# Kernel optimization log

Hardware: AMD Instinct MI355X
Metric: run time of the kernel (lower is better)

## Reference

```python
import jax, jax.numpy as jnp
import numpy as np

IMAGE_SIZE = 256
PSIZE = 6
STRIDE = 2
WINDOW = IMAGE_SIZE + 1 - PSIZE  # 251
CUR = np.arange(0, WINDOW, STRIDE)
if CUR[-1] != WINDOW - 1:
    CUR = np.concatenate([CUR, np.array([WINDOW - 1])])
NPOS = len(CUR)  # 126 strided window positions per axis
BATCH = 128


def setup_inputs() -> dict:
    key = jax.random.key(0)
    x = jax.random.normal(key, (BATCH, 1, IMAGE_SIZE, IMAGE_SIZE), dtype=jnp.float32)
    return {"x": x}


def reference(x):
    # Equivalent to patch_tf.forward(to_patch): for each strided window position
    # (r, c) in CUR x CUR and each in-patch offset (i, j) in [0, PSIZE)^2,
    # output[b, r*NPOS + c, i*PSIZE + j] = x[b, 0, r + i, c + j].
    cur = jnp.asarray(CUR, dtype=jnp.int32)          # [NPOS]
    off = jnp.arange(PSIZE, dtype=jnp.int32)         # [PSIZE]
    row_idx = cur[:, None] + off[None, :]            # [NPOS, PSIZE]
    col_idx = cur[:, None] + off[None, :]            # [NPOS, PSIZE]
    img = x[:, 0]                                    # [B, H, W]
    # Advanced-index gather -> [B, NPOS, NPOS, PSIZE, PSIZE]
    patches = img[:, row_idx[:, None, :, None], col_idx[None, :, None, :]]
    return patches.reshape(x.shape[0], NPOS * NPOS, PSIZE * PSIZE)
```

## Files before the change

kernel.cpp:

```cpp
#include <hip/hip_runtime.h>


#define IMG 256
#define PSZ 6
#define NPOS 126
#define BATCHN 128
#define PATCH_ELEMS (PSZ * PSZ)
#define PER_BATCH (NPOS * NPOS * PATCH_ELEMS)
#define TOTAL_ELEMS (BATCHN * PER_BATCH)
#define TOTAL_VEC4 (TOTAL_ELEMS / 4)

__global__ __launch_bounds__(256) void image2patch_kernel(
    const float* __restrict__ x, float* __restrict__ out) {
  const int tid4 = blockIdx.x * blockDim.x + threadIdx.x;
  const int flat = tid4 * 4;

  const int b   = flat / PER_BATCH;
  const int rem = flat - b * PER_BATCH;
  const int p   = rem / PATCH_ELEMS;
  const int k   = rem - p * PATCH_ELEMS;
  const int i   = p / NPOS;
  const int j   = p - i * NPOS;

  const float* img = x + (size_t)b * (IMG * IMG) + (2 * i) * IMG + (2 * j);

  float4 v;
  {
    int kk = k;     int r = kk / PSZ, c = kk - PSZ * r; v.x = img[r * IMG + c];
    kk = k + 1;     r = kk / PSZ;     c = kk - PSZ * r; v.y = img[r * IMG + c];
    kk = k + 2;     r = kk / PSZ;     c = kk - PSZ * r; v.z = img[r * IMG + c];
    kk = k + 3;     r = kk / PSZ;     c = kk - PSZ * r; v.w = img[r * IMG + c];
  }
  reinterpret_cast<float4*>(out)[tid4] = v;
}

extern "C" void kernel_launch(void* const* d_in, const int* in_sizes, int n_in,
                              void* d_out, int out_size, void* d_ws, size_t ws_size,
                              hipStream_t stream) {
  const float* x = (const float*)d_in[0];
  float* out = (float*)d_out;
  image2patch_kernel<<<TOTAL_VEC4 / 256, 256, 0, stream>>>(x, out);
}
```

Baseline: 357.9 us.

## Stage six-row image band in LDS per output row and gather patches from shared memory

Each block now handles one (batch, window-row) pair and cooperatively loads the six input rows it needs into padded shared memory using vectorized float4 loads. Patch elements are then gathered from LDS and written as contiguous float4 stores. This replaces redundant scattered global reads with one coalesced band load per block. It adds a barrier and LDS traffic, and the per-block work no longer divides evenly among the threads.

```diff
diff --git a/kernel.cpp b/kernel.cpp
--- a/kernel.cpp
+++ b/kernel.cpp
@@ -5,33 +5,42 @@
 #define PSZ 6
 #define NPOS 126
 #define BATCHN 128
-#define PATCH_ELEMS (PSZ * PSZ)
-#define PER_BATCH (NPOS * NPOS * PATCH_ELEMS)
-#define TOTAL_ELEMS (BATCHN * PER_BATCH)
-#define TOTAL_VEC4 (TOTAL_ELEMS / 4)
+#define LDSW 257
+#define VECS_PER_BAND 1134
 
 __global__ __launch_bounds__(256) void image2patch_kernel(
     const float* __restrict__ x, float* __restrict__ out) {
-  const int tid4 = blockIdx.x * blockDim.x + threadIdx.x;
-  const int flat = tid4 * 4;
+  __shared__ float tile[PSZ * LDSW];
 
-  const int b   = flat / PER_BATCH;
-  const int rem = flat - b * PER_BATCH;
-  const int p   = rem / PATCH_ELEMS;
-  const int k   = rem - p * PATCH_ELEMS;
-  const int i   = p / NPOS;
-  const int j   = p - i * NPOS;
+  const int blk = blockIdx.x;
+  const int b = blk / NPOS;
+  const int i = blk - b * NPOS;
+  const int t = threadIdx.x;
 
-  const float* img = x + (size_t)b * (IMG * IMG) + (2 * i) * IMG + (2 * j);
+  const float* src = x + (size_t)b * (IMG * IMG) + (size_t)(2 * i) * IMG;
+  for (int idx = t; idx < PSZ * (IMG / 4); idx += 256) {
+    const int row  = idx >> 6;
+    const int col4 = idx & 63;
+    float4 v = reinterpret_cast<const float4*>(src + row * IMG)[col4];
+    float* d = &tile[row * LDSW + col4 * 4];
+    d[0] = v.x; d[1] = v.y; d[2] = v.z; d[3] = v.w;
+  }
+  __syncthreads();
 
-  float4 v;
-  {
-    int kk = k;     int r = kk / PSZ, c = kk - PSZ * r; v.x = img[r * IMG + c];
-    kk = k + 1;     r = kk / PSZ;     c = kk - PSZ * r; v.y = img[r * IMG + c];
-    kk = k + 2;     r = kk / PSZ;     c = kk - PSZ * r; v.z = img[r * IMG + c];
-    kk = k + 3;     r = kk / PSZ;     c = kk - PSZ * r; v.w = img[r * IMG + c];
+  float4* outp = reinterpret_cast<float4*>(
+      out + ((size_t)b * (NPOS * NPOS) + (size_t)i * NPOS) * (PSZ * PSZ));
+  for (int q = t; q < VECS_PER_BAND; q += 256) {
+    const int f  = q * 4;
+    const int j  = f / 36;
+    const int k0 = f - j * 36;
+    const int jj = 2 * j;
+    float4 v;
+    { const int k = k0;     const int r = k / PSZ, c = k - PSZ * r; v.x = tile[r * LDSW + jj + c]; }
+    { const int k = k0 + 1; const int r = k / PSZ, c = k - PSZ * r; v.y = tile[r * LDSW + jj + c]; }
+    { const int k = k0 + 2; const int r = k / PSZ, c = k - PSZ * r; v.z = tile[r * LDSW + jj + c]; }
+    { const int k = k0 + 3; const int r = k / PSZ, c = k - PSZ * r; v.w = tile[r * LDSW + jj + c]; }
+    outp[q] = v;
   }
-  reinterpret_cast<float4*>(out)[tid4] = v;
 }
 
 extern "C" void kernel_launch(void* const* d_in, const int* in_sizes, int n_in,
@@ -39,5 +48,5 @@
                               hipStream_t stream) {
   const float* x = (const float*)d_in[0];
   float* out = (float*)d_out;
-  image2patch_kernel<<<TOTAL_VEC4 / 256, 256, 0, stream>>>(x, out);
+  image2patch_kernel<<<BATCHN * NPOS, 256, 0, stream>>>(x, out);
 }
```

Result: faster. 313.7 us (-12.3%).
